# Optimization experiments

Measured on AMD Instinct MI355X. Metric: run time of the kernel, lower is better.

The kernel has to match this reference:

```python
import jax, jax.numpy as jnp
import numpy as np

N_NODES = 50000
N_EDGES = 800000
D_FEAT = 64
UNITS = 64


def setup_inputs() -> dict:
    key = jax.random.key(0)
    k1, k2, k3, k4, k5 = jax.random.split(key, 5)
    node_feat = jax.random.normal(k1, (N_NODES, D_FEAT), dtype=jnp.float32)
    edge_feat = jax.random.normal(k2, (N_EDGES, D_FEAT), dtype=jnp.float32)
    src_idx = jax.random.randint(k3, (N_EDGES,), 0, N_NODES)
    tgt_idx = jax.random.randint(k4, (N_EDGES,), 0, N_NODES)
    # Dense kernel for the edge update: concat(src, tgt, edge) -> units
    W = jax.random.normal(k5, (3 * D_FEAT, UNITS), dtype=jnp.float32) / np.sqrt(3 * D_FEAT)
    b = jnp.zeros((UNITS,), dtype=jnp.float32)
    return {"node_feat": node_feat, "edge_feat": edge_feat,
            "src_idx": src_idx, "tgt_idx": tgt_idx, "W": W, "b": b}


def reference(node_feat, edge_feat, src_idx, tgt_idx, W, b):
    # EdgeSetUpdate: gather endpoint states, concat with edge feature, Dense+relu.
    # [n_edges, 3*d_feat]
    msg_in = jnp.concatenate([node_feat[src_idx], node_feat[tgt_idx], edge_feat], axis=-1)
    messages = jax.nn.relu(msg_in @ W + b)  # [n_edges, units]
    # pool_edges_to_node(..., TARGET, 'sum'): segment-sum messages to target nodes.
    pooled = jax.ops.segment_sum(messages, tgt_idx, num_segments=node_feat.shape[0])
    return pooled
```

## Files before the change

kernel.cpp:

```cpp
#include <hip/hip_runtime.h>
#include <hip/hip_bf16.h>


using s16x8 = __attribute__((ext_vector_type(8))) short;
using f32x4 = __attribute__((ext_vector_type(4))) float;

#define WT_LD 200

static __device__ __forceinline__ ushort f2bf(float f) {
    union { __hip_bfloat16 h; ushort u; } cv;
    cv.h = __float2bfloat16(f);
    return cv.u;
}
static __device__ __forceinline__ float bf2f(ushort u) {
    union { unsigned u; float f; } cv;
    cv.u = ((unsigned)u) << 16;
    return cv.f;
}

__global__ void prep_wt(const float* __restrict__ W, ushort* __restrict__ WT) {
    int idx = blockIdx.x * blockDim.x + threadIdx.x;
    if (idx < 64 * 192) {
        int n = idx / 192, k = idx % 192;
        WT[idx] = f2bf(W[k * 64 + n]);
    }
}

__global__ void hist_tgt(const int* __restrict__ tgt, int* __restrict__ counts, int n_edges) {
    int i = blockIdx.x * blockDim.x + threadIdx.x;
    if (i < n_edges) atomicAdd(&counts[tgt[i]], 1);
}

__global__ __launch_bounds__(1024) void scan_counts(
    const int* __restrict__ counts, int* __restrict__ offsets, int* __restrict__ woff,
    int n_nodes, int n_edges)
{
    __shared__ int wsum[16];
    __shared__ int base_s;
    const int tid = threadIdx.x, lane = tid & 63, wid = tid >> 6;
    if (tid == 0) base_s = 0;
    __syncthreads();
    for (int c0 = 0; c0 < n_nodes; c0 += 1024) {
        const int idx = c0 + tid;
        const int v = (idx < n_nodes) ? counts[idx] : 0;
        int x = v;
#pragma unroll
        for (int o = 1; o < 64; o <<= 1) { int t = __shfl_up(x, o, 64); if (lane >= o) x += t; }
        if (lane == 63) wsum[wid] = x;
        __syncthreads();
        if (tid < 16) {
            int w = wsum[tid];
#pragma unroll
            for (int o = 1; o < 16; o <<= 1) { int t = __shfl_up(w, o, 16); if (tid >= o) w += t; }
            wsum[tid] = w;
        }
        __syncthreads();
        const int wbase = (wid == 0) ? 0 : wsum[wid - 1];
        const int excl = base_s + wbase + x - v;
        if (idx < n_nodes) { offsets[idx] = excl; woff[idx] = excl; }
        const int total = wsum[15];
        __syncthreads();
        if (tid == 0) base_s += total;
        __syncthreads();
    }
    if (threadIdx.x == 0) offsets[n_nodes] = n_edges;
}

__global__ void build_rank(const int* __restrict__ tgt, int* __restrict__ woff,
                           int* __restrict__ rank, int n_edges) {
    int i = blockIdx.x * blockDim.x + threadIdx.x;
    if (i < n_edges) {
        rank[i] = atomicAdd(&woff[tgt[i]], 1);
    }
}

__global__ __launch_bounds__(256, 4) void edge_gemm_pipe(
    const float* __restrict__ node, const float* __restrict__ edgef,
    const int* __restrict__ src, const int* __restrict__ tgt,
    const int* __restrict__ rank,
    const ushort* __restrict__ WT, const float* __restrict__ bias,
    ushort* __restrict__ msg, int n_edges)
{
    __shared__ __align__(16) ushort WTs[64][WT_LD];
    __shared__ __align__(16) ushort T[4][16][72];

    const int wave = threadIdx.x >> 6, lane = threadIdx.x & 63;
    const int g = lane >> 4, r = lane & 15;

    for (int c = threadIdx.x; c < 1536; c += 256) {
        const int row = c / 24, col = (c % 24) * 8;
        *reinterpret_cast<s16x8*>(&WTs[row][col]) =
            *reinterpret_cast<const s16x8*>(WT + row * 192 + col);
    }
    float bv[4];
#pragma unroll
    for (int nt = 0; nt < 4; ++nt) bv[nt] = bias[nt * 16 + r];
    __syncthreads();

    const int ntiles = (n_edges + 15) >> 4;
    const int nw = gridDim.x << 2;
    int t = blockIdx.x * 4 + wave;
    if (t >= ntiles) return;

    auto posof = [&](int tt) { int p = tt * 16 + r; return (p < n_edges) ? p : n_edges - 1; };

    int p = posof(t);
    int si = src[p], ti = tgt[p];
    f32x4 lo[6], hi[6];
    {
        const float* b0 = node + (size_t)si * 64;
        const float* b1 = node + (size_t)ti * 64;
        const float* b2 = edgef + (size_t)p * 64;
#pragma unroll
        for (int ks = 0; ks < 6; ++ks) {
            const float* bb = (ks < 2) ? b0 : (ks < 4) ? b1 : b2;
            const float* pp = bb + (ks & 1) * 32 + g * 8;
            lo[ks] = *reinterpret_cast<const f32x4*>(pp);
            hi[ks] = *reinterpret_cast<const f32x4*>(pp + 4);
        }
    }
    int pN = posof(t + nw);
    int siN = src[pN], tiN = tgt[pN];
    s16x8 A[6];
#pragma unroll
    for (int ks = 0; ks < 6; ++ks)
#pragma unroll
        for (int j = 0; j < 4; ++j) { A[ks][j] = (short)f2bf(lo[ks][j]); A[ks][4 + j] = (short)f2bf(hi[ks][j]); }

    while (true) {
        const bool have_next = (t + nw) < ntiles;
        if (have_next) {
            const float* b0 = node + (size_t)siN * 64;
            const float* b1 = node + (size_t)tiN * 64;
            const float* b2 = edgef + (size_t)pN * 64;
#pragma unroll
            for (int ks = 0; ks < 6; ++ks) {
                const float* bb = (ks < 2) ? b0 : (ks < 4) ? b1 : b2;
                const float* pp = bb + (ks & 1) * 32 + g * 8;
                lo[ks] = *reinterpret_cast<const f32x4*>(pp);
                hi[ks] = *reinterpret_cast<const f32x4*>(pp + 4);
            }
        }
        const int pN2 = posof(t + 2 * nw);
        const int siN2 = src[pN2], tiN2 = tgt[pN2];

        int lz;
        asm volatile("v_mov_b32 %0, 0" : "=v"(lz));
        const ushort* wbase = &WTs[0][0] + lz;
        f32x4 acc[4] = {{0.f,0.f,0.f,0.f},{0.f,0.f,0.f,0.f},{0.f,0.f,0.f,0.f},{0.f,0.f,0.f,0.f}};
#pragma unroll
        for (int ks = 0; ks < 6; ++ks)
#pragma unroll
            for (int nt = 0; nt < 4; ++nt) {
                const s16x8 bf = *reinterpret_cast<const s16x8*>(
                    wbase + (nt * 16 + r) * WT_LD + ks * 32 + g * 8);
                acc[nt] = __builtin_amdgcn_mfma_f32_16x16x32_bf16(A[ks], bf, acc[nt], 0, 0, 0);
            }

        const int tile0 = t * 16;
#pragma unroll
        for (int nt = 0; nt < 4; ++nt)
#pragma unroll
            for (int j = 0; j < 4; ++j)
                T[wave][g * 4 + j][nt * 16 + r] = f2bf(fmaxf(acc[nt][j] + bv[nt], 0.0f));
        asm volatile("s_waitcnt lgkmcnt(0)" ::: "memory");
        {
            const int row = lane >> 2, q = lane & 3;
            if (tile0 + row < n_edges) {
                const int rk = rank[tile0 + row];
                const s16x8 m0 = *reinterpret_cast<const s16x8*>(&T[wave][row][q * 16]);
                const s16x8 m1 = *reinterpret_cast<const s16x8*>(&T[wave][row][q * 16 + 8]);
                const size_t op = (size_t)rk * 64 + q * 16;
                *reinterpret_cast<s16x8*>(msg + op) = m0;
                *reinterpret_cast<s16x8*>(msg + op + 8) = m1;
            }
        }

        if (!have_next) break;
        t += nw;
#pragma unroll
        for (int ks = 0; ks < 6; ++ks)
#pragma unroll
            for (int j = 0; j < 4; ++j) { A[ks][j] = (short)f2bf(lo[ks][j]); A[ks][4 + j] = (short)f2bf(hi[ks][j]); }
        pN = pN2; siN = siN2; tiN = tiN2;
    }
}

__global__ __launch_bounds__(256) void pool_seq(
    const ushort* __restrict__ msg, const int* __restrict__ offsets,
    float* __restrict__ out, int n_nodes)
{
    const int wave = threadIdx.x >> 6, lane = threadIdx.x & 63;
    const int n = blockIdx.x * 4 + wave;
    if (n >= n_nodes) return;
    const int s = offsets[n], e = offsets[n + 1];
    const int c = lane & 7;
    const int rg = lane >> 3;
    float acc[8] = {0.f,0.f,0.f,0.f,0.f,0.f,0.f,0.f};
    for (int i = s + rg; i < e; i += 8) {
        const s16x8 v = *reinterpret_cast<const s16x8*>(msg + (size_t)i * 64 + c * 8);
#pragma unroll
        for (int j = 0; j < 8; ++j) acc[j] += bf2f((ushort)v[j]);
    }
#pragma unroll
    for (int j = 0; j < 8; ++j) {
        acc[j] += __shfl_xor(acc[j], 8, 64);
        acc[j] += __shfl_xor(acc[j], 16, 64);
        acc[j] += __shfl_xor(acc[j], 32, 64);
    }
    if (rg == 0) {
        const f32x4 o0 = {acc[0], acc[1], acc[2], acc[3]};
        const f32x4 o1 = {acc[4], acc[5], acc[6], acc[7]};
        *reinterpret_cast<f32x4*>(out + (size_t)n * 64 + c * 8) = o0;
        *reinterpret_cast<f32x4*>(out + (size_t)n * 64 + c * 8 + 4) = o1;
    }
}

__global__ __launch_bounds__(256) void edge_gemm_atomic(
    const float* __restrict__ node, const float* __restrict__ edgef,
    const int* __restrict__ src, const int* __restrict__ tgt,
    const ushort* __restrict__ WT, const float* __restrict__ bias,
    float* __restrict__ out, int n_edges)
{
    const int lane = threadIdx.x & 63;
    const int g = lane >> 4, r = lane & 15;
    const int tile0 = blockIdx.x * 64 + (threadIdx.x >> 6) * 16;
    int pos = tile0 + r; if (pos >= n_edges) pos = n_edges - 1;
    const int si = src[pos], ti = tgt[pos];
    const float* base0 = node + (size_t)si * 64;
    const float* base1 = node + (size_t)ti * 64;
    const float* base2 = edgef + (size_t)pos * 64;
    f32x4 acc[4] = {{0.f,0.f,0.f,0.f},{0.f,0.f,0.f,0.f},{0.f,0.f,0.f,0.f},{0.f,0.f,0.f,0.f}};
#pragma unroll
    for (int ks = 0; ks < 6; ++ks) {
        const float* b = (ks < 2) ? base0 : (ks < 4) ? base1 : base2;
        const float* p = b + (ks & 1) * 32 + g * 8;
        const f32x4 lo = *reinterpret_cast<const f32x4*>(p);
        const f32x4 hi = *reinterpret_cast<const f32x4*>(p + 4);
        s16x8 a;
#pragma unroll
        for (int j = 0; j < 4; ++j) { a[j] = (short)f2bf(lo[j]); a[4 + j] = (short)f2bf(hi[j]); }
#pragma unroll
        for (int nt = 0; nt < 4; ++nt) {
            const s16x8 bf = *reinterpret_cast<const s16x8*>(WT + (nt * 16 + r) * 192 + ks * 32 + g * 8);
            acc[nt] = __builtin_amdgcn_mfma_f32_16x16x32_bf16(a, bf, acc[nt], 0, 0, 0);
        }
    }
#pragma unroll
    for (int nt = 0; nt < 4; ++nt) {
        const float bv = bias[nt * 16 + r];
#pragma unroll
        for (int j = 0; j < 4; ++j) {
            const int e = tile0 + g * 4 + j;
            if (e < n_edges) {
                float v = fmaxf(acc[nt][j] + bv, 0.0f);
                unsafeAtomicAdd(out + (size_t)tgt[e] * 64 + nt * 16 + r, v);
            }
        }
    }
}

extern "C" void kernel_launch(void* const* d_in, const int* in_sizes, int n_in,
                              void* d_out, int out_size, void* d_ws, size_t ws_size,
                              hipStream_t stream) {
    const float* node  = (const float*)d_in[0];
    const float* edgef = (const float*)d_in[1];
    const int*   src   = (const int*)d_in[2];
    const int*   tgt   = (const int*)d_in[3];
    const float* W     = (const float*)d_in[4];
    const float* bias  = (const float*)d_in[5];
    float* out = (float*)d_out;
    const int n_edges = in_sizes[2];
    const int n_nodes = in_sizes[0] / 64;

    char* ws = (char*)d_ws;
    size_t cur = 0;
    auto take = [&](size_t b) { size_t s = cur; cur = (cur + b + 255) & ~(size_t)255; return s; };
    const size_t oWT   = take((size_t)64 * 192 * 2);
    const size_t oCnt  = take((size_t)n_nodes * 4);
    const size_t oOff  = take((size_t)(n_nodes + 1) * 4);
    const size_t oWoff = take((size_t)n_nodes * 4);
    const size_t oRank = take((size_t)n_edges * 4);
    const size_t oMsg  = take((size_t)n_edges * 64 * 2);
    const bool sorted_ok = (cur <= ws_size);

    ushort* WT = (ushort*)(ws + oWT);
    prep_wt<<<48, 256, 0, stream>>>(W, WT);

    if (sorted_ok) {
        int* counts  = (int*)(ws + oCnt);
        int* offsets = (int*)(ws + oOff);
        int* woff    = (int*)(ws + oWoff);
        int* rank    = (int*)(ws + oRank);
        ushort* msg  = (ushort*)(ws + oMsg);

        hipMemsetAsync(counts, 0, (size_t)n_nodes * 4, stream);
        hist_tgt<<<(n_edges + 255) / 256, 256, 0, stream>>>(tgt, counts, n_edges);
        scan_counts<<<1, 1024, 0, stream>>>(counts, offsets, woff, n_nodes, n_edges);
        build_rank<<<(n_edges + 255) / 256, 256, 0, stream>>>(tgt, woff, rank, n_edges);

        const int ntiles = (n_edges + 15) / 16;
        int blocks = 1024;
        if (blocks * 4 > ntiles) blocks = (ntiles + 3) / 4;
        edge_gemm_pipe<<<blocks, 256, 0, stream>>>(
            node, edgef, src, tgt, rank, WT, bias, msg, n_edges);
        pool_seq<<<(n_nodes + 3) / 4, 256, 0, stream>>>(msg, offsets, out, n_nodes);
    } else {
        hipMemsetAsync(d_out, 0, (size_t)out_size * sizeof(float), stream);
        edge_gemm_atomic<<<(n_edges + 63) / 64, 256, 0, stream>>>(
            node, edgef, src, tgt, WT, bias, out, n_edges);
    }
}
```

Baseline: 486.0 us.

## Use 1024-thread blocks, XOR-swizzle weight LDS, prefetch rank indices

Grows the edge GEMM block from 4 to 16 waves so the weight tile loaded into LDS is shared by more waves and fewer blocks repeat that load. The padded weight layout becomes an unpadded one with an XOR swizzle on 16-byte slots to avoid LDS bank conflicts. The rank index used for the scattered message store is now loaded one iteration ahead alongside the feature prefetch. The risk is that launch_bounds(1024,6) and the larger LDS footprint limit registers and occupancy, which could cause spills or leave fewer waves resident per CU.

Measured after the change: 621.7 us. 1.28x slower.

```diff
diff --git a/kernel.cpp b/kernel.cpp
--- a/kernel.cpp
+++ b/kernel.cpp
@@ -4,8 +4,6 @@
 
 using s16x8 = __attribute__((ext_vector_type(8))) short;
 using f32x4 = __attribute__((ext_vector_type(4))) float;
-
-#define WT_LD 200
 
 static __device__ __forceinline__ ushort f2bf(float f) {
     union { __hip_bfloat16 h; ushort u; } cv;
@@ -74,23 +72,25 @@
     }
 }
 
-__global__ __launch_bounds__(256, 4) void edge_gemm_pipe(
+__global__ __launch_bounds__(1024, 6) void edge_gemm_pipe(
     const float* __restrict__ node, const float* __restrict__ edgef,
     const int* __restrict__ src, const int* __restrict__ tgt,
     const int* __restrict__ rank,
     const ushort* __restrict__ WT, const float* __restrict__ bias,
     ushort* __restrict__ msg, int n_edges)
 {
-    __shared__ __align__(16) ushort WTs[64][WT_LD];
-    __shared__ __align__(16) ushort T[4][16][72];
+    __shared__ __align__(16) ushort WTs[64 * 192];
+    __shared__ __align__(16) ushort T[16][16][72];
 
     const int wave = threadIdx.x >> 6, lane = threadIdx.x & 63;
     const int g = lane >> 4, r = lane & 15;
-
-    for (int c = threadIdx.x; c < 1536; c += 256) {
-        const int row = c / 24, col = (c % 24) * 8;
-        *reinterpret_cast<s16x8*>(&WTs[row][col]) =
-            *reinterpret_cast<const s16x8*>(WT + row * 192 + col);
+    const int erow = lane >> 2, q = lane & 3;
+
+    for (int c = threadIdx.x; c < 1536; c += 1024) {
+        const int row = c / 24, slot = c % 24;
+        const int sl = (slot & 24) | ((slot & 7) ^ (row & 7));
+        *reinterpret_cast<s16x8*>(&WTs[row * 192 + sl * 8]) =
+            *reinterpret_cast<const s16x8*>(WT + row * 192 + slot * 8);
     }
     float bv[4];
 #pragma unroll
@@ -98,14 +98,16 @@
     __syncthreads();
 
     const int ntiles = (n_edges + 15) >> 4;
-    const int nw = gridDim.x << 2;
-    int t = blockIdx.x * 4 + wave;
+    const int nw = gridDim.x << 4;
+    int t = blockIdx.x * 16 + wave;
     if (t >= ntiles) return;
 
     auto posof = [&](int tt) { int p = tt * 16 + r; return (p < n_edges) ? p : n_edges - 1; };
+    auto rposof = [&](int tt) { int p = tt * 16 + erow; return (p < n_edges) ? p : n_edges - 1; };
 
     int p = posof(t);
     int si = src[p], ti = tgt[p];
+    int rkC = rank[rposof(t)];
     f32x4 lo[6], hi[6];
     {
         const float* b0 = node + (size_t)si * 64;
@@ -129,6 +131,7 @@
 
     while (true) {
         const bool have_next = (t + nw) < ntiles;
+        int rkN = 0;
         if (have_next) {
             const float* b0 = node + (size_t)siN * 64;
             const float* b1 = node + (size_t)tiN * 64;
@@ -140,20 +143,23 @@
                 lo[ks] = *reinterpret_cast<const f32x4*>(pp);
                 hi[ks] = *reinterpret_cast<const f32x4*>(pp + 4);
             }
+            rkN = rank[rposof(t + nw)];
         }
         const int pN2 = posof(t + 2 * nw);
         const int siN2 = src[pN2], tiN2 = tgt[pN2];
 
         int lz;
         asm volatile("v_mov_b32 %0, 0" : "=v"(lz));
-        const ushort* wbase = &WTs[0][0] + lz;
+        const ushort* wbase = &WTs[0] + lz;
         f32x4 acc[4] = {{0.f,0.f,0.f,0.f},{0.f,0.f,0.f,0.f},{0.f,0.f,0.f,0.f},{0.f,0.f,0.f,0.f}};
 #pragma unroll
         for (int ks = 0; ks < 6; ++ks)
 #pragma unroll
             for (int nt = 0; nt < 4; ++nt) {
+                const int slot = ks * 4 + g;
+                const int sl = (slot & 24) | ((slot & 7) ^ (r & 7));
                 const s16x8 bf = *reinterpret_cast<const s16x8*>(
-                    wbase + (nt * 16 + r) * WT_LD + ks * 32 + g * 8);
+                    wbase + (nt * 16 + r) * 192 + sl * 8);
                 acc[nt] = __builtin_amdgcn_mfma_f32_16x16x32_bf16(A[ks], bf, acc[nt], 0, 0, 0);
             }
 
@@ -164,16 +170,12 @@
             for (int j = 0; j < 4; ++j)
                 T[wave][g * 4 + j][nt * 16 + r] = f2bf(fmaxf(acc[nt][j] + bv[nt], 0.0f));
         asm volatile("s_waitcnt lgkmcnt(0)" ::: "memory");
-        {
-            const int row = lane >> 2, q = lane & 3;
-            if (tile0 + row < n_edges) {
-                const int rk = rank[tile0 + row];
-                const s16x8 m0 = *reinterpret_cast<const s16x8*>(&T[wave][row][q * 16]);
-                const s16x8 m1 = *reinterpret_cast<const s16x8*>(&T[wave][row][q * 16 + 8]);
-                const size_t op = (size_t)rk * 64 + q * 16;
-                *reinterpret_cast<s16x8*>(msg + op) = m0;
-                *reinterpret_cast<s16x8*>(msg + op + 8) = m1;
-            }
+        if (tile0 + erow < n_edges) {
+            const s16x8 m0 = *reinterpret_cast<const s16x8*>(&T[wave][erow][q * 16]);
+            const s16x8 m1 = *reinterpret_cast<const s16x8*>(&T[wave][erow][q * 16 + 8]);
+            const size_t op = (size_t)rkC * 64 + q * 16;
+            *reinterpret_cast<s16x8*>(msg + op) = m0;
+            *reinterpret_cast<s16x8*>(msg + op + 8) = m1;
         }
 
         if (!have_next) break;
@@ -182,6 +184,7 @@
         for (int ks = 0; ks < 6; ++ks)
 #pragma unroll
             for (int j = 0; j < 4; ++j) { A[ks][j] = (short)f2bf(lo[ks][j]); A[ks][4 + j] = (short)f2bf(hi[ks][j]); }
+        rkC = rkN;
         pN = pN2; siN = siN2; tiN = tiN2;
     }
 }
@@ -300,9 +303,9 @@
         build_rank<<<(n_edges + 255) / 256, 256, 0, stream>>>(tgt, woff, rank, n_edges);
 
         const int ntiles = (n_edges + 15) / 16;
-        int blocks = 1024;
-        if (blocks * 4 > ntiles) blocks = (ntiles + 3) / 4;
-        edge_gemm_pipe<<<blocks, 256, 0, stream>>>(
+        int blocks = 512;
+        if (blocks * 16 > ntiles) blocks = (ntiles + 15) / 16;
+        edge_gemm_pipe<<<blocks, 1024, 0, stream>>>(
             node, edgef, src, tgt, rank, WT, bias, msg, n_edges);
         pool_seq<<<(n_nodes + 3) / 4, 256, 0, stream>>>(msg, offsets, out, n_nodes);
     } else {
```
